# Kernel tuning notes

Hardware: AMD Instinct MI355X
Metric: run time of the kernel (lower is better)

## Reference

```python
import jax, jax.numpy as jnp
import numpy as np

NUM_USERS = 8192
NUM_ITEMS = 32768
FEAT_DIM = 129  # args.feat_dim + 1 (Hyperboloid time coordinate)
C = 1.0         # curvature args.c
EPS = 1e-7      # hgcn Hyperboloid eps for float32
MAX_SQDIST = 50.0


def setup_inputs() -> dict:
    key = jax.random.key(0)
    h = jax.random.normal(key, (NUM_USERS + NUM_ITEMS, FEAT_DIM), dtype=jnp.float32)
    return {"h": h}


def _predict(h):
    # Hyperboloid.sqdist(x, y, c):
    #   K = 1/c
    #   prod = -x0*y0 + sum_{d>=1} x_d*y_d   (Minkowski inner product)
    #   theta = clamp(-prod / K, min=1+eps)
    #   sqdist = clamp(K * arccosh(theta)^2, max=50)
    # predict() returns -sqdist for every (user, item) pair.
    hu = h[:NUM_USERS]                     # [U, D]
    hi = h[NUM_USERS:NUM_USERS + NUM_ITEMS]  # [I, D]
    signs = jnp.concatenate(
        [-jnp.ones((1,), h.dtype), jnp.ones((FEAT_DIM - 1,), h.dtype)]
    )
    # One GEMM computes all Minkowski dots (replaces per-user Python loop)
    prod = jnp.einsum('ud,id->ui', hu, hi * signs)   # [U, I]
    K = 1.0 / C
    theta = jnp.maximum(-prod / K, 1.0 + EPS)
    sqdist = jnp.minimum(K * jnp.arccosh(theta) ** 2, MAX_SQDIST)
    return -sqdist


def reference(h):
    return _predict(h)
```

## Files before the change

kernel.cpp:

```cpp
#include <hip/hip_runtime.h>
#include <hip/hip_bf16.h>

#define NUM_USERS 8192
#define NUM_ITEMS 32768
#define FEAT 129
#define KP 160
#define NOUT 32768

typedef _Float16 f16x8 __attribute__((ext_vector_type(8)));
typedef float    f32x4 __attribute__((ext_vector_type(4)));

__global__ void pack_kernel(const float* __restrict__ h,
                            _Float16* __restrict__ apack,
                            _Float16* __restrict__ bpack) {
    int idx = blockIdx.x * blockDim.x + threadIdx.x;
    int row = idx / KP;
    int col = idx - row * KP;
    float v = 0.0f;
    if (col < FEAT) v = h[(size_t)row * FEAT + col];
    if (row < NUM_USERS) {
        if (col == 0) v = -v;
        apack[(size_t)row * KP + col] = (_Float16)v;
    } else {
        bpack[(size_t)(row - NUM_USERS) * KP + col] = (_Float16)v;
    }
}

__global__ __launch_bounds__(256) void gemm_arccosh_kernel(
        const _Float16* __restrict__ A,
        const _Float16* __restrict__ B,
        float* __restrict__ out) {
    __shared__ __align__(16) _Float16 As[128 * 32];
    __shared__ __align__(16) _Float16 Bs[128 * 32];

    const int t  = threadIdx.x;
    const int l  = t & 63;
    const int w  = t >> 6;
    const int wm = (w >> 1) * 64;
    const int wn = (w & 1)  * 64;
    const int q  = l >> 4;
    const int lm = l & 15;

    const int mBase = blockIdx.y * 128;
    const int nBase = blockIdx.x * 128;

    f32x4 acc[4][4];
#pragma unroll
    for (int i = 0; i < 4; i++)
#pragma unroll
        for (int j = 0; j < 4; j++) acc[i][j] = (f32x4){0.f, 0.f, 0.f, 0.f};

    for (int k0 = 0; k0 < KP; k0 += 32) {
#pragma unroll
        for (int i = 0; i < 2; i++) {
            const int o   = i * 4096 + t * 16;
            const int row = o >> 6;
            const int kc  = (o >> 4) & 3;
            const _Float16* ga = A + (size_t)(mBase + row) * KP + k0 + kc * 8;
            __builtin_amdgcn_global_load_lds(
                (const __attribute__((address_space(1))) unsigned int*)ga,
                (__attribute__((address_space(3))) unsigned int*)((char*)As + o),
                16, 0, 0);
            const _Float16* gb = B + (size_t)(nBase + row) * KP + k0 + kc * 8;
            __builtin_amdgcn_global_load_lds(
                (const __attribute__((address_space(1))) unsigned int*)gb,
                (__attribute__((address_space(3))) unsigned int*)((char*)Bs + o),
                16, 0, 0);
        }
        __syncthreads();

        f16x8 af[4], bf[4];
#pragma unroll
        for (int im = 0; im < 4; im++)
            af[im] = *(const f16x8*)&As[(wm + im * 16 + lm) * 32 + q * 8];
#pragma unroll
        for (int in = 0; in < 4; in++)
            bf[in] = *(const f16x8*)&Bs[(wn + in * 16 + lm) * 32 + q * 8];

#pragma unroll
        for (int im = 0; im < 4; im++)
#pragma unroll
            for (int in = 0; in < 4; in++)
                acc[im][in] = __builtin_amdgcn_mfma_f32_16x16x32_f16(
                    af[im], bf[in], acc[im][in], 0, 0, 0);
        __syncthreads();
    }

#pragma unroll
    for (int im = 0; im < 4; im++) {
#pragma unroll
        for (int in = 0; in < 4; in++) {
            const int n = nBase + wn + in * 16 + lm;
#pragma unroll
            for (int r = 0; r < 4; r++) {
                const int m = mBase + wm + im * 16 + q * 4 + r;
                const float prod  = acc[im][in][r];
                const float theta = fmaxf(-prod, 1.0f + 1e-7f);
                const float t2    = fmaxf(__builtin_fmaf(theta, theta, -1.0f), 0.0f);
                const float ac    = __logf(theta + __builtin_sqrtf(t2));
                const float s     = fminf(ac * ac, 50.0f);
                out[(size_t)m * NOUT + n] = -s;
            }
        }
    }
}

extern "C" void kernel_launch(void* const* d_in, const int* in_sizes, int n_in,
                              void* d_out, int out_size, void* d_ws, size_t ws_size,
                              hipStream_t stream) {
    const float* h = (const float*)d_in[0];
    float* out = (float*)d_out;

    _Float16* apack = (_Float16*)d_ws;
    _Float16* bpack = apack + (size_t)NUM_USERS * KP;

    const int total = (NUM_USERS + NUM_ITEMS) * KP;
    pack_kernel<<<total / 256, 256, 0, stream>>>(h, apack, bpack);

    dim3 grid(NUM_ITEMS / 128, NUM_USERS / 128);
    gemm_arccosh_kernel<<<grid, 256, 0, stream>>>(apack, bpack, out);
}
```

Baseline: 1.253 ms.

## Preload full K into LDS, swap MFMA operands for vectorized nontemporal stores, remap blocks

The kernel now loads the whole K=160 slice of both tiles into LDS at once, which removes the per-k-step barriers. It swaps the MFMA operand order so each lane holds four consecutive output columns and can write them with one 16-byte nontemporal store instead of scattered scalar stores. Blocks move to a 1D grid with a swizzled mapping that groups tiles for L2 reuse, and launch bounds now request two blocks per CU. The cost is 80KB of LDS per block, which may limit occupancy.

```diff
diff --git a/kernel.cpp b/kernel.cpp
--- a/kernel.cpp
+++ b/kernel.cpp
@@ -1,5 +1,4 @@
 #include <hip/hip_runtime.h>
-#include <hip/hip_bf16.h>
 
 #define NUM_USERS 8192
 #define NUM_ITEMS 32768
@@ -26,12 +25,12 @@
     }
 }
 
-__global__ __launch_bounds__(256) void gemm_arccosh_kernel(
+__global__ __launch_bounds__(256, 2) void gemm_arccosh_kernel(
         const _Float16* __restrict__ A,
         const _Float16* __restrict__ B,
         float* __restrict__ out) {
-    __shared__ __align__(16) _Float16 As[128 * 32];
-    __shared__ __align__(16) _Float16 Bs[128 * 32];
+    __shared__ __align__(16) _Float16 As[5 * 128 * 32];
+    __shared__ __align__(16) _Float16 Bs[5 * 128 * 32];
 
     const int t  = threadIdx.x;
     const int l  = t & 63;
@@ -41,8 +40,31 @@
     const int q  = l >> 4;
     const int lm = l & 15;
 
-    const int mBase = blockIdx.y * 128;
-    const int nBase = blockIdx.x * 128;
+    const int bid = blockIdx.x;
+    const int seq = bid >> 3;
+    const int nBase = (((bid & 7) << 5) + (seq & 31)) << 7;
+    const int mBase = (seq >> 5) << 7;
+
+#pragma unroll
+    for (int i = 0; i < 10; i++) {
+        const int ob   = i * 4096 + t * 16;
+        const int ks   = ob >> 13;
+        const int orem = ob & 8191;
+        const int row  = orem >> 6;
+        const int kc   = (orem >> 4) & 3;
+        const int koff = ks * 32 + kc * 8;
+        const _Float16* ga = A + (size_t)(mBase + row) * KP + koff;
+        __builtin_amdgcn_global_load_lds(
+            (const __attribute__((address_space(1))) unsigned int*)ga,
+            (__attribute__((address_space(3))) unsigned int*)((char*)As + ob),
+            16, 0, 0);
+        const _Float16* gb = B + (size_t)(nBase + row) * KP + koff;
+        __builtin_amdgcn_global_load_lds(
+            (const __attribute__((address_space(1))) unsigned int*)gb,
+            (__attribute__((address_space(3))) unsigned int*)((char*)Bs + ob),
+            16, 0, 0);
+    }
+    __syncthreads();
 
     f32x4 acc[4][4];
 #pragma unroll
@@ -50,57 +72,39 @@
 #pragma unroll
         for (int j = 0; j < 4; j++) acc[i][j] = (f32x4){0.f, 0.f, 0.f, 0.f};
 
-    for (int k0 = 0; k0 < KP; k0 += 32) {
 #pragma unroll
-        for (int i = 0; i < 2; i++) {
-            const int o   = i * 4096 + t * 16;
-            const int row = o >> 6;
-            const int kc  = (o >> 4) & 3;
-            const _Float16* ga = A + (size_t)(mBase + row) * KP + k0 + kc * 8;
-            __builtin_amdgcn_global_load_lds(
-                (const __attribute__((address_space(1))) unsigned int*)ga,
-                (__attribute__((address_space(3))) unsigned int*)((char*)As + o),
-                16, 0, 0);
-            const _Float16* gb = B + (size_t)(nBase + row) * KP + k0 + kc * 8;
-            __builtin_amdgcn_global_load_lds(
-                (const __attribute__((address_space(1))) unsigned int*)gb,
-                (__attribute__((address_space(3))) unsigned int*)((char*)Bs + o),
-                16, 0, 0);
-        }
-        __syncthreads();
-
+    for (int ks = 0; ks < 5; ks++) {
         f16x8 af[4], bf[4];
 #pragma unroll
         for (int im = 0; im < 4; im++)
-            af[im] = *(const f16x8*)&As[(wm + im * 16 + lm) * 32 + q * 8];
+            af[im] = *(const f16x8*)&As[ks * 4096 + (wm + im * 16 + lm) * 32 + q * 8];
 #pragma unroll
         for (int in = 0; in < 4; in++)
-            bf[in] = *(const f16x8*)&Bs[(wn + in * 16 + lm) * 32 + q * 8];
-
+            bf[in] = *(const f16x8*)&Bs[ks * 4096 + (wn + in * 16 + lm) * 32 + q * 8];
 #pragma unroll
         for (int im = 0; im < 4; im++)
 #pragma unroll
             for (int in = 0; in < 4; in++)
                 acc[im][in] = __builtin_amdgcn_mfma_f32_16x16x32_f16(
-                    af[im], bf[in], acc[im][in], 0, 0, 0);
-        __syncthreads();
+                    bf[in], af[im], acc[im][in], 0, 0, 0);
     }
 
 #pragma unroll
     for (int im = 0; im < 4; im++) {
+        float* orow = out + (size_t)(mBase + wm + im * 16 + lm) * NOUT;
 #pragma unroll
         for (int in = 0; in < 4; in++) {
-            const int n = nBase + wn + in * 16 + lm;
+            f32x4 v;
 #pragma unroll
             for (int r = 0; r < 4; r++) {
-                const int m = mBase + wm + im * 16 + q * 4 + r;
                 const float prod  = acc[im][in][r];
                 const float theta = fmaxf(-prod, 1.0f + 1e-7f);
                 const float t2    = fmaxf(__builtin_fmaf(theta, theta, -1.0f), 0.0f);
                 const float ac    = __logf(theta + __builtin_sqrtf(t2));
-                const float s     = fminf(ac * ac, 50.0f);
-                out[(size_t)m * NOUT + n] = -s;
+                v[r] = fmaxf(-(ac * ac), -50.0f);
             }
+            __builtin_nontemporal_store(
+                v, (f32x4*)(orow + (nBase + wn + in * 16 + q * 4)));
         }
     }
 }
@@ -117,6 +121,6 @@
     const int total = (NUM_USERS + NUM_ITEMS) * KP;
     pack_kernel<<<total / 256, 256, 0, stream>>>(h, apack, bpack);
 
-    dim3 grid(NUM_ITEMS / 128, NUM_USERS / 128);
-    gemm_arccosh_kernel<<<grid, 256, 0, stream>>>(apack, bpack, out);
+    const int nblocks = (NUM_ITEMS / 128) * (NUM_USERS / 128);
+    gemm_arccosh_kernel<<<nblocks, 256, 0, stream>>>(apack, bpack, out);
 }
```

Result: faster. 1.164 ms (-7.2%).
